# Optimization experiments

Hardware: AMD Instinct MI355X
Metric: run time of the kernel (lower is better)

The kernel has to match this reference:

```python
import jax, jax.numpy as jnp
import numpy as np

B, R, C = 2, 64, 256
PH = PW = 7
KMAX = 8            # max pool-kernel size per axis given roi size bounds (kernel<=7 here)
HW = [160, 80, 40, 20]   # FPN level spatial sizes for a 640px image, strides 4/8/16/32
STRIDES = [4.0, 8.0, 16.0, 32.0]
TOP = 224.0         # config.top_pyramid_roi_size
HIDDEN = 2048
NCLS = 20
SCALE = float(np.round(np.sqrt(C), 2))  # np.round(sqrt(inner_dim),2) in SelfAttention


def setup_inputs() -> dict:
    key = jax.random.key(0)
    ks = jax.random.split(key, 32)
    U = lambda k, s, lo, hi: jax.random.uniform(k, s, minval=lo, maxval=hi)
    x1 = U(ks[0], (B, R), 0.0, 260.0)
    y1 = U(ks[1], (B, R), 0.0, 260.0)
    w = U(ks[2], (B, R), 16.0, 360.0)
    h = U(ks[3], (B, R), 16.0, 360.0)
    rois = jnp.stack([x1, y1, jnp.minimum(x1 + w, 639.0), jnp.minimum(y1 + h, 639.0)], -1)
    N = lambda k, s, sc: (sc * jax.random.normal(k, s)).astype(jnp.float32)
    inp = {'rois': rois}
    for i in range(4):
        inp[f'fm{i}'] = N(ks[4 + i], (B, C, HW[i], HW[i]), 1.0)
    inp['wq'] = N(ks[8], (C, C), 0.02);  inp['bq'] = jnp.zeros((C,), jnp.float32)
    inp['wk'] = N(ks[9], (C, C), 0.02);  inp['bk'] = jnp.zeros((C,), jnp.float32)
    inp['wv'] = N(ks[10], (C, C), 0.02); inp['bv'] = jnp.zeros((C,), jnp.float32)
    inp['wo'] = N(ks[11], (C, C), 0.02); inp['bo'] = jnp.zeros((C,), jnp.float32)
    inp['w1'] = N(ks[12], (C * PH * PW, HIDDEN), 0.02); inp['b1'] = jnp.zeros((HIDDEN,), jnp.float32)
    inp['w2'] = N(ks[13], (HIDDEN, HIDDEN), 0.02);       inp['b2'] = jnp.zeros((HIDDEN,), jnp.float32)
    inp['wreg'] = N(ks[14], (HIDDEN, 4 * (NCLS + 1)), 0.02); inp['breg'] = jnp.zeros((4 * (NCLS + 1),), jnp.float32)
    inp['wcls'] = N(ks[15], (HIDDEN, NCLS + 1), 0.02);       inp['bcls'] = jnp.zeros((NCLS + 1,), jnp.float32)
    return inp


def _forward(rois, fm0, fm1, fm2, fm3, wq, bq, wk, bk, wv, bv, wo, bo,
             w1, b1, w2, b2, wreg, breg, wcls, bcls):
    Hmax = HW[0]
    pad = lambda fm: jnp.pad(fm, ((0, 0), (0, 0), (0, Hmax - fm.shape[-2]), (0, Hmax - fm.shape[-1])))
    feats = jnp.stack([pad(fm0), pad(fm1), pad(fm2), pad(fm3)])  # [4,B,C,Hmax,Hmax]
    heights = jnp.array(HW, jnp.int32)
    strides = jnp.array(STRIDES, jnp.float32)

    r = rois.reshape(-1, 4)                 # [N,4] xyxy in pixels
    Nroi = r.shape[0]
    bidx = jnp.repeat(jnp.arange(B, dtype=jnp.int32), R)
    size = jnp.sqrt((r[:, 2] - r[:, 0]) * (r[:, 3] - r[:, 1]))
    # int() truncates toward zero, then clamp(0,3) -- matches torch
    lvl = jnp.clip((3.0 + jnp.log(size / TOP)).astype(jnp.int32), 0, 3)
    s = strides[lvl]
    x1 = (r[:, 0] / s).astype(jnp.int32); y1 = (r[:, 1] / s).astype(jnp.int32)
    x2 = (r[:, 2] / s).astype(jnp.int32); y2 = (r[:, 3] / s).astype(jnp.int32)
    Hl = heights[lvl]                        # per-roi level map size (square maps)

    def expand(lo, hi, cap, pool):
        # replicate the symmetric while-loop expansion until span >= pool
        for _ in range(pool):
            need = (hi - lo + 1) < pool
            lo = jnp.where(need, jnp.maximum(lo - 1, 0), lo)
            hi = jnp.where(need, jnp.minimum(hi + 1, cap - 1), hi)
        return lo, hi

    y1, y2 = expand(y1, y2, Hl, PH)
    x1, x2 = expand(x1, x2, Hl, PW)
    rh = y2 - y1 + 1; rw = x2 - x1 + 1
    kh = (rh + PH - 1) // PH; sh = rh // PH   # ceil / floor kernel & stride
    kw = (rw + PW - 1) // PW; sw = rw // PW

    ar_p = jnp.arange(PH); ar_k = jnp.arange(KMAX)

    def pool_one(l, b, yy, xx, kh_, kw_, sh_, sw_):
        rows = jnp.clip(yy + ar_p[:, None] * sh_ + ar_k[None, :], 0, Hmax - 1)  # [PH,K]
        cols = jnp.clip(xx + ar_p[:, None] * sw_ + ar_k[None, :], 0, Hmax - 1)  # [PW,K]
        patch = feats[l, b][:, rows[:, :, None, None], cols[None, None, :, :]]  # [C,PH,K,PW,K]
        m = (ar_k < kh_)[:, None, None] & (ar_k < kw_)[None, None, :]           # [K,1,K] -> bcast
        patch = jnp.where(m, patch, -jnp.inf)
        return patch.max(axis=(2, 4))                                           # [C,PH,PW]

    pooled = jax.vmap(pool_one)(lvl, bidx, y1, x1, kh, kw, sh, sw)  # [N,C,PH,PW]

    # SelfAttention over the PH*PW spatial tokens of each ROI
    L = PH * PW
    tok = pooled.reshape(Nroi, C, L).transpose(0, 2, 1)            # [N,L,C]
    q = tok @ wq + bq
    k = tok @ wk + bk
    v = tok @ wv + bv
    att = jax.nn.softmax(jnp.einsum('nlc,nmc->nlm', q, k) / SCALE, axis=-1)
    ctx = jnp.einsum('nlm,nmc->nlc', att, v) @ wo + bo             # [N,L,C]
    x = pooled.reshape(Nroi, C, L) + ctx.transpose(0, 2, 1)        # residual add
    x = x.reshape(Nroi, C * L)

    h1 = jax.nn.relu(x @ w1 + b1)
    h2 = jax.nn.relu(h1 @ w2 + b2)
    bbox_reg = h2 @ wreg + breg                                    # [N, 4*(NCLS+1)]
    bbox_classes = jax.nn.softmax(h2 @ wcls + bcls, axis=-1)       # [N, NCLS+1]
    return bbox_reg, bbox_classes


def reference(rois, fm0, fm1, fm2, fm3, wq, bq, wk, bk, wv, bv, wo, bo,
              w1, b1, w2, b2, wreg, breg, wcls, bcls):
    return _forward(rois, fm0, fm1, fm2, fm3, wq, bq, wk, bk, wv, bv, wo, bo,
                    w1, b1, w2, b2, wreg, breg, wcls, bcls)
```

## Files before the change

### kernel.cpp

```cpp
#include <hip/hip_runtime.h>
#include <hip/hip_bf16.h>
#include <stdint.h>

typedef __attribute__((ext_vector_type(8))) short bf16x8;
typedef __attribute__((ext_vector_type(4))) float f32x4;

__device__ __forceinline__ float blo(unsigned u){ union{float f;unsigned x;}v; v.x = u<<16; return v.f; }
__device__ __forceinline__ float bhi(unsigned u){ union{float f;unsigned x;}v; v.x = u & 0xFFFF0000u; return v.f; }
__device__ __forceinline__ unsigned short f2bf(float f){
  union{float f;unsigned x;}v; v.f=f; unsigned x=v.x;
  return (unsigned short)((x + 0x7fffu + ((x>>16)&1u)) >> 16);
}
__device__ __forceinline__ unsigned cvtpk(float lo, float hi){
  unsigned r;
  asm("v_cvt_pk_bf16_f32 %0, %1, %2" : "=v"(r) : "v"(lo), "v"(hi));
  return r;
}
__device__ __forceinline__ void gll16(const float* g, float* l){
  __builtin_amdgcn_global_load_lds(
      (const __attribute__((address_space(1))) unsigned int*)g,
      (__attribute__((address_space(3))) unsigned int*)l, 16, 0, 0);
}

__global__ __launch_bounds__(256) void pool_pack_kernel(
    const float* __restrict__ rois,
    const float* __restrict__ fm0, const float* __restrict__ fm1,
    const float* __restrict__ fm2, const float* __restrict__ fm3,
    float* __restrict__ pooled, unsigned short* __restrict__ tok,
    const float* __restrict__ wreg, const float* __restrict__ wcls, float* __restrict__ wT)
{
  int bx = blockIdx.x;
  int tid = threadIdx.x;
  if (bx >= 896){
    int c = bx - 896;
    if (c < 84){
      for (int k = tid; k < 2048; k += 256) wT[(size_t)c*2048 + k] = wreg[(size_t)k*84 + c];
    } else {
      int cc = c - 84;
      for (int k = tid; k < 2048; k += 256) wT[(size_t)c*2048 + k] = wcls[(size_t)k*21 + cc];
    }
    return;
  }
  int n = bx / 7;
  int ph = bx - n*7;
  int c = tid;
  const float* r = rois + n*4;
  int b = n >> 6;
  float rx1=r[0], ry1=r[1], rx2=r[2], ry2=r[3];
  float size = sqrtf((rx2-rx1)*(ry2-ry1));
  int lvl = (int)(3.0f + logf(size/224.0f));
  if (lvl < 0) lvl = 0; if (lvl > 3) lvl = 3;
  const float strides_[4] = {4.f,8.f,16.f,32.f};
  const int hw_[4] = {160,80,40,20};
  float s = strides_[lvl]; int Hl = hw_[lvl];
  int x1 = (int)(rx1/s), y1 = (int)(ry1/s), x2 = (int)(rx2/s), y2 = (int)(ry2/s);
  #pragma unroll
  for (int it=0; it<7; ++it){
    bool need = (y2-y1+1) < 7;
    if (need){ y1 = (y1-1 > 0) ? y1-1 : 0; y2 = (y2+1 < Hl-1) ? y2+1 : Hl-1; }
  }
  #pragma unroll
  for (int it=0; it<7; ++it){
    bool need = (x2-x1+1) < 7;
    if (need){ x1 = (x1-1 > 0) ? x1-1 : 0; x2 = (x2+1 < Hl-1) ? x2+1 : Hl-1; }
  }
  int rh = y2-y1+1, rw = x2-x1+1;
  int kh = (rh+6)/7, sh = rh/7, kw = (rw+6)/7, sw2 = rw/7;
  const float* fm = (lvl==0)?fm0:(lvl==1)?fm1:(lvl==2)?fm2:fm3;
  const float* fp = fm + ((size_t)(b*256 + c))*(size_t)(Hl*Hl);
  int r0 = y1 + ph*sh;
  for (int pw=0; pw<7; ++pw){
    int c0 = x1 + pw*sw2;
    float m = -3.4e38f;
    for (int i=0;i<kh;++i){
      const float* rp = fp + (size_t)(r0+i)*Hl + c0;
      for (int j=0;j<kw;++j) m = fmaxf(m, rp[j]);
    }
    int l = ph*7+pw;
    pooled[((size_t)n*49 + l)*256 + c] = m;
    tok[((size_t)n*49 + l)*256 + c] = f2bf(m);
  }
}

template<bool GATHER>
__global__ __launch_bounds__(256) void fc_kernel(
    const unsigned short* __restrict__ A, const float* __restrict__ B,
    float* __restrict__ outf, int M, int K, int kChunk)
{
  __shared__ __align__(16) float Bs[4][32][64];
  int bid = blockIdx.x;
  int pe = gridDim.x >> 3;
  bid = (bid & 7)*pe + (bid >> 3);
  const int per = 64;
  int kc = bid / per;
  int rem = bid - kc*per;
  int bm = rem & 1, bn = rem >> 1;
  int m0 = bm*64, n0 = bn*64;
  int tid = threadIdx.x, lane = tid & 63, wave = tid >> 6;
  int wm = wave & 1, wn = wave >> 1;
  int g = lane >> 4, c = lane & 15;
  int k0 = kc*kChunk;
  int nSteps = kChunk >> 5;

  f32x4 acc[2][2];
  #pragma unroll
  for (int i=0;i<2;++i)
    #pragma unroll
    for (int j=0;j<2;++j){ acc[i][j][0]=0.f; acc[i][j][1]=0.f; acc[i][j][2]=0.f; acc[i][j][3]=0.f; }

  int rowInWave = lane >> 4;
  int colOff = n0 + (lane & 15)*4;
  const unsigned short* Ap0 = A + (size_t)(m0 + wm*32 +      c)*K + g*8;
  const unsigned short* Ap1 = A + (size_t)(m0 + wm*32 + 16 + c)*K + g*8;

  auto srcRow = [&](int k)->const float*{
    if constexpr (GATHER){ int kk = k; return B + ((size_t)((kk & 255)*49 + (kk >> 8)))*2048; }
    else                 { return B + (size_t)k*2048; }
  };
  auto stage = [&](int buf, int kk){
    int r0a = kk + wave*8 + rowInWave;
    int r0b = r0a + 4;
    gll16(srcRow(r0a) + colOff, &Bs[buf][wave*8    ][0]);
    gll16(srcRow(r0b) + colOff, &Bs[buf][wave*8 + 4][0]);
  };

  stage(0, k0); stage(1, k0+32); stage(2, k0+64);
  uint4 aCur0 = *(const uint4*)(Ap0 + k0);
  uint4 aCur1 = *(const uint4*)(Ap1 + k0);

  for (int i = 0; i < nSteps; ++i){
    int kk = k0 + (i<<5);
    int pend = nSteps - i;
    if (pend >= 3)      asm volatile("s_waitcnt vmcnt(4)" ::: "memory");
    else if (pend == 2) asm volatile("s_waitcnt vmcnt(2)" ::: "memory");
    else                asm volatile("s_waitcnt vmcnt(0)" ::: "memory");
    __builtin_amdgcn_s_barrier();

    uint4 aNxt0 = aCur0, aNxt1 = aCur1;
    if (i+1 < nSteps){
      aNxt0 = *(const uint4*)(Ap0 + kk + 32);
      aNxt1 = *(const uint4*)(Ap1 + kk + 32);
    }
    if (i+3 < nSteps) stage((i+3)&3, kk + 96);

    const float* fb = &Bs[i&3][g*8][wn*32 + c];
    float q0f[8], q1f[8];
    #pragma unroll
    for (int j=0;j<8;++j){ q0f[j] = fb[j*64]; q1f[j] = fb[j*64 + 16]; }
    union { unsigned u[4]; bf16x8 v; } q0u, q1u;
    q0u.u[0]=cvtpk(q0f[0],q0f[1]); q0u.u[1]=cvtpk(q0f[2],q0f[3]);
    q0u.u[2]=cvtpk(q0f[4],q0f[5]); q0u.u[3]=cvtpk(q0f[6],q0f[7]);
    q1u.u[0]=cvtpk(q1f[0],q1f[1]); q1u.u[1]=cvtpk(q1f[2],q1f[3]);
    q1u.u[2]=cvtpk(q1f[4],q1f[5]); q1u.u[3]=cvtpk(q1f[6],q1f[7]);
    bf16x8 f0 = *(const bf16x8*)&aCur0;
    bf16x8 f1 = *(const bf16x8*)&aCur1;
    acc[0][0] = __builtin_amdgcn_mfma_f32_16x16x32_bf16(f0,q0u.v,acc[0][0],0,0,0);
    acc[0][1] = __builtin_amdgcn_mfma_f32_16x16x32_bf16(f0,q1u.v,acc[0][1],0,0,0);
    acc[1][0] = __builtin_amdgcn_mfma_f32_16x16x32_bf16(f1,q0u.v,acc[1][0],0,0,0);
    acc[1][1] = __builtin_amdgcn_mfma_f32_16x16x32_bf16(f1,q1u.v,acc[1][1],0,0,0);
    aCur0 = aNxt0; aCur1 = aNxt1;
  }

  int rq = g << 2;
  #pragma unroll
  for (int mr=0;mr<2;++mr){
    #pragma unroll
    for (int nc=0;nc<2;++nc){
      int rowb = m0 + wm*32 + mr*16 + rq;
      int colM = n0 + wn*32 + nc*16 + c;
      #pragma unroll
      for (int r2=0;r2<4;++r2){
        outf[(size_t)kc*M*2048 + (size_t)(rowb+r2)*2048 + colM] = acc[mr][nc][r2];
      }
    }
  }
}

template<int EPI>
__global__ __launch_bounds__(256) void gemm_kernel(
    const unsigned short* __restrict__ A,
    const float* __restrict__ B0, const float* __restrict__ B1, const float* __restrict__ B2,
    const float* __restrict__ bias0, const float* __restrict__ bias1, const float* __restrict__ bias2,
    unsigned short* __restrict__ o0, unsigned short* __restrict__ o1, unsigned short* __restrict__ o2,
    const float* __restrict__ pooled,
    int M, int Nper, int K, int nM, int nN, int kChunk)
{
  __shared__ __align__(16) unsigned short Bs[2][2048];
  int bid = blockIdx.x;
  int tid = threadIdx.x;
  int per = nM*nN;
  int kc  = bid / per;
  int rem = bid - kc*per;
  int bm = rem % nM, bn = rem / nM;
  int m0 = bm*64, n0 = bn*64;
  int mat = n0 / Nper;
  int col0 = n0 - mat*Nper;
  const float* Bp    = (mat==0)?B0:(mat==1)?B1:B2;
  const float* biasp = (mat==0)?bias0:(mat==1)?bias1:bias2;
  unsigned short* outp = (mat==0)?o0:(mat==1)?o1:o2;
  int k0 = kc*kChunk;
  int nMacro = kChunk >> 7;
  int lane = tid & 63, wave = tid >> 6;
  int wm = wave & 1, wn = wave >> 1;
  int g = lane >> 4, c = lane & 15;

  f32x4 acc[2][2];
  #pragma unroll
  for (int i=0;i<2;++i)
    #pragma unroll
    for (int j=0;j<2;++j){ acc[i][j][0]=0.f; acc[i][j][1]=0.f; acc[i][j][2]=0.f; acc[i][j][3]=0.f; }

  int brow = tid >> 3, bcg = tid & 7;
  int bw_idx = brow*64 + ((bcg*8) ^ ((brow>>3)<<4));
  const float* Bbase = Bp + (size_t)brow*Nper + col0 + bcg*8;
  int rb0 = g*512 + (((wn*2  )^g)*16 + c);
  int rb1 = g*512 + (((wn*2+1)^g)*16 + c);
  const unsigned short* Ap0 = A + (size_t)(m0 + wm*32 +      c)*K + g*8;
  const unsigned short* Ap1 = A + (size_t)(m0 + wm*32 + 16 + c)*K + g*8;

  auto writeB = [&](int buf, const float4& bx, const float4& by){
    uint4 w;
    w.x = cvtpk(bx.x,bx.y); w.y = cvtpk(bx.z,bx.w);
    w.z = cvtpk(by.x,by.y); w.w = cvtpk(by.z,by.w);
    *(uint4*)&Bs[buf][bw_idx] = w;
  };
  auto readFrags = [&](int buf, bf16x8& r0, bf16x8& r1){
    union { unsigned short s[8]; bf16x8 v; } u0, u1;
    const unsigned short* bsp = &Bs[buf][0];
    #pragma unroll
    for (int j=0;j<8;++j){ u0.s[j] = bsp[rb0 + j*64]; u1.s[j] = bsp[rb1 + j*64]; }
    r0 = u0.v; r1 = u1.v;
  };
  auto mfma4 = [&](const bf16x8& f0, const bf16x8& f1, const bf16x8& q0, const bf16x8& q1){
    acc[0][0] = __builtin_amdgcn_mfma_f32_16x16x32_bf16(f0,q0,acc[0][0],0,0,0);
    acc[0][1] = __builtin_amdgcn_mfma_f32_16x16x32_bf16(f0,q1,acc[0][1],0,0,0);
    acc[1][0] = __builtin_amdgcn_mfma_f32_16x16x32_bf16(f1,q0,acc[1][0],0,0,0);
    acc[1][1] = __builtin_amdgcn_mfma_f32_16x16x32_bf16(f1,q1,acc[1][1],0,0,0);
  };

  for (int mi = 0; mi < nMacro; ++mi){
    int kk = k0 + (mi << 7);
    uint4 a0x = *(const uint4*)(Ap0+kk),    a0y = *(const uint4*)(Ap1+kk);
    uint4 a1x = *(const uint4*)(Ap0+kk+32), a1y = *(const uint4*)(Ap1+kk+32);
    uint4 a2x = *(const uint4*)(Ap0+kk+64), a2y = *(const uint4*)(Ap1+kk+64);
    uint4 a3x = *(const uint4*)(Ap0+kk+96), a3y = *(const uint4*)(Ap1+kk+96);
    const float* p0 = Bbase + (size_t)kk*Nper;
    const float* p1 = p0 + (size_t)32*Nper;
    const float* p2 = p0 + (size_t)64*Nper;
    const float* p3 = p0 + (size_t)96*Nper;
    float4 b0a = *(const float4*)p0, b0b = *(const float4*)(p0+4);
    float4 b1a = *(const float4*)p1, b1b = *(const float4*)(p1+4);
    float4 b2a = *(const float4*)p2, b2b = *(const float4*)(p2+4);
    float4 b3a = *(const float4*)p3, b3b = *(const float4*)(p3+4);

    writeB(0, b0a, b0b);
    __syncthreads();
    bf16x8 q0,q1;
    readFrags(0,q0,q1);
    writeB(1,b1a,b1b);
    mfma4(*(const bf16x8*)&a0x, *(const bf16x8*)&a0y, q0,q1);
    __syncthreads();
    readFrags(1,q0,q1);
    writeB(0,b2a,b2b);
    mfma4(*(const bf16x8*)&a1x, *(const bf16x8*)&a1y, q0,q1);
    __syncthreads();
    readFrags(0,q0,q1);
    writeB(1,b3a,b3b);
    mfma4(*(const bf16x8*)&a2x, *(const bf16x8*)&a2y, q0,q1);
    __syncthreads();
    readFrags(1,q0,q1);
    mfma4(*(const bf16x8*)&a3x, *(const bf16x8*)&a3y, q0,q1);
  }

  int rq = g << 2, cl = c;
  #pragma unroll
  for (int mr=0;mr<2;++mr){
    #pragma unroll
    for (int nc=0;nc<2;++nc){
      int rowb = m0 + wm*32 + mr*16 + rq;
      int colM = col0 + wn*32 + nc*16 + cl;
      #pragma unroll
      for (int r2=0;r2<4;++r2){
        float v = acc[mr][nc][r2];
        int rr = rowb + r2;
        if constexpr (EPI==0){
          v += biasp[colM];
          outp[(size_t)rr*Nper + colM] = f2bf(v);
        } else {
          v += biasp[colM];
          v += pooled[(size_t)rr*256 + colM];
          int nn = rr/49, l = rr - nn*49;
          outp[(size_t)nn*12544 + l*256 + colM] = f2bf(v);
        }
      }
    }
  }
}

__global__ __launch_bounds__(256) void reduce1_kernel(
    const float* __restrict__ part, const float* __restrict__ b1,
    unsigned short* __restrict__ h1, int nPart)
{
  int i = blockIdx.x*256 + threadIdx.x;
  float4 s = ((const float4*)part)[i];
  for (int kc = 1; kc < nPart; ++kc){
    float4 p = ((const float4*)part)[(size_t)kc*65536 + i];
    s.x += p.x; s.y += p.y; s.z += p.z; s.w += p.w;
  }
  float4 bb = *(const float4*)(b1 + ((i<<2) & 2047));
  s.x = fmaxf(s.x+bb.x,0.f); s.y = fmaxf(s.y+bb.y,0.f);
  s.z = fmaxf(s.z+bb.z,0.f); s.w = fmaxf(s.w+bb.w,0.f);
  uint2 w;
  w.x = cvtpk(s.x, s.y); w.y = cvtpk(s.z, s.w);
  *(uint2*)&h1[(size_t)i<<2] = w;
}

__global__ __launch_bounds__(256) void reduce2_kernel(
    const float* __restrict__ part, float* __restrict__ h2f, int nPart)
{
  int i = blockIdx.x*256 + threadIdx.x;
  float4 s = ((const float4*)part)[i];
  for (int kc = 1; kc < nPart; ++kc){
    float4 p = ((const float4*)part)[(size_t)kc*65536 + i];
    s.x += p.x; s.y += p.y; s.z += p.z; s.w += p.w;
  }
  ((float4*)h2f)[i] = s;
}

__global__ __launch_bounds__(256) void attn_kernel(
    const unsigned short* __restrict__ Q, const unsigned short* __restrict__ Km,
    const unsigned short* __restrict__ V, unsigned short* __restrict__ ctx)
{
  int n = blockIdx.x, half = blockIdx.y, tid = threadIdx.x;
  int r0 = half*25, rcnt = half ? 24 : 25;
  __shared__ __align__(16) unsigned short qs[25*256];
  __shared__ __align__(16) unsigned short ks[49*260];
  __shared__ float S[25*49];
  const uint4* qg = (const uint4*)(Q + ((size_t)n*49 + r0)*256);
  for (int i = tid; i < rcnt*32; i += 256) ((uint4*)qs)[i] = qg[i];
  const uint2* kg = (const uint2*)(Km + (size_t)n*49*256);
  for (int i = tid; i < 49*64; i += 256){
    int j = i >> 6, s = i & 63;
    *(uint2*)(ks + j*260 + s*4) = kg[i];
  }
  __syncthreads();
  for (int p = tid; p < rcnt*49; p += 256){
    int i = p/49, j = p - i*49;
    const uint2* qr = (const uint2*)(qs + i*256);
    const uint2* kr = (const uint2*)(ks + j*260);
    float sum = 0.f;
    #pragma unroll 8
    for (int c4 = 0; c4 < 64; ++c4){
      uint2 qv = qr[c4], kv = kr[c4];
      sum += blo(qv.x)*blo(kv.x) + bhi(qv.x)*bhi(kv.x);
      sum += blo(qv.y)*blo(kv.y) + bhi(qv.y)*bhi(kv.y);
    }
    S[p] = sum * (1.0f/16.0f);
  }
  __syncthreads();
  const uint2* vg = (const uint2*)(V + (size_t)n*49*256);
  for (int i = tid; i < 49*64; i += 256){
    int j = i >> 6, s = i & 63;
    *(uint2*)(ks + j*260 + s*4) = vg[i];
  }
  if (tid < rcnt){
    float* row = S + tid*49;
    float mx = row[0];
    for (int j=1;j<49;++j) mx = fmaxf(mx,row[j]);
    float sm = 0.f;
    for (int j=0;j<49;++j){ float e = expf(row[j]-mx); row[j]=e; sm+=e; }
    float inv = 1.0f/sm;
    for (int j=0;j<49;++j) row[j] *= inv;
  }
  __syncthreads();
  for (int idx = tid; idx < rcnt*64; idx += 256){
    int i = idx >> 6, cp4 = idx & 63;
    const float* att = S + i*49;
    float s0=0.f, s1=0.f, s2=0.f, s3=0.f;
    #pragma unroll 7
    for (int j=0;j<49;++j){
      uint2 v = *(const uint2*)(ks + j*260 + cp4*4);
      float a = att[j];
      s0 += a*blo(v.x); s1 += a*bhi(v.x);
      s2 += a*blo(v.y); s3 += a*bhi(v.y);
    }
    uint2 outw;
    outw.x = (unsigned)f2bf(s0) | ((unsigned)f2bf(s1) << 16);
    outw.y = (unsigned)f2bf(s2) | ((unsigned)f2bf(s3) << 16);
    *(uint2*)&ctx[((size_t)n*49 + r0 + i)*256 + cp4*4] = outw;
  }
}

__global__ __launch_bounds__(256) void heads_dot(
    const float* __restrict__ h2f, const float* __restrict__ b2,
    const float* __restrict__ wT,
    const float* __restrict__ breg, const float* __restrict__ bcls,
    float* __restrict__ out, float* __restrict__ logits)
{
  int gw = (blockIdx.x*256 + threadIdx.x) >> 6;
  int lane = threadIdx.x & 63;
  int m = gw / 105, c = gw - m*105;
  const float4* hp = (const float4*)(h2f + (size_t)m*2048);
  const float4* bp = (const float4*)b2;
  const float4* wp = (const float4*)(wT + (size_t)c*2048);
  float sum = 0.f;
  #pragma unroll
  for (int i=0;i<8;++i){
    float4 a = hp[i*64 + lane];
    float4 bb = bp[i*64 + lane];
    float4 w = wp[i*64 + lane];
    sum += fmaxf(a.x+bb.x,0.f)*w.x + fmaxf(a.y+bb.y,0.f)*w.y
         + fmaxf(a.z+bb.z,0.f)*w.z + fmaxf(a.w+bb.w,0.f)*w.w;
  }
  #pragma unroll
  for (int off=32; off; off>>=1) sum += __shfl_down(sum, off, 64);
  if (lane == 0){
    if (c < 84) out[(size_t)m*84 + c] = sum + breg[c];
    else        logits[(size_t)m*21 + (c-84)] = sum + bcls[c-84];
  }
}

__global__ __launch_bounds__(128) void cls_softmax(
    const float* __restrict__ logits, float* __restrict__ out)
{
  int m = threadIdx.x;
  const float* lg = logits + (size_t)m*21;
  float mx = lg[0];
  #pragma unroll
  for (int j=1;j<21;++j) mx = fmaxf(mx, lg[j]);
  float sm = 0.f;
  float e[21];
  #pragma unroll
  for (int j=0;j<21;++j){ e[j] = expf(lg[j]-mx); sm += e[j]; }
  float inv = 1.0f/sm;
  #pragma unroll
  for (int j=0;j<21;++j) out[10752 + (size_t)m*21 + j] = e[j]*inv;
}

extern "C" void kernel_launch(void* const* d_in, const int* in_sizes, int n_in,
                              void* d_out, int out_size, void* d_ws, size_t ws_size,
                              hipStream_t stream)
{
  (void)in_sizes; (void)n_in; (void)out_size; (void)ws_size;
  const float* rois = (const float*)d_in[0];
  const float* fm0  = (const float*)d_in[1];
  const float* fm1  = (const float*)d_in[2];
  const float* fm2  = (const float*)d_in[3];
  const float* fm3  = (const float*)d_in[4];
  const float* wq   = (const float*)d_in[5];
  const float* bq   = (const float*)d_in[6];
  const float* wk   = (const float*)d_in[7];
  const float* bk   = (const float*)d_in[8];
  const float* wv   = (const float*)d_in[9];
  const float* bv   = (const float*)d_in[10];
  const float* wo   = (const float*)d_in[11];
  const float* bo   = (const float*)d_in[12];
  const float* w1   = (const float*)d_in[13];
  const float* b1   = (const float*)d_in[14];
  const float* w2   = (const float*)d_in[15];
  const float* b2   = (const float*)d_in[16];
  const float* wreg = (const float*)d_in[17];
  const float* breg = (const float*)d_in[18];
  const float* wcls = (const float*)d_in[19];
  const float* bcls = (const float*)d_in[20];
  float* out = (float*)d_out;

  char* ws = (char*)d_ws;
  float*          pooled = (float*)(ws + 0);
  unsigned short* tok    = (unsigned short*)(ws + 6422528);
  unsigned short* Qb     = (unsigned short*)(ws + 9633792);
  unsigned short* Kb     = (unsigned short*)(ws + 12845056);
  unsigned short* Vb     = (unsigned short*)(ws + 16056320);
  unsigned short* ctx    = (unsigned short*)(ws + 19267584);
  unsigned short* xb     = (unsigned short*)(ws + 22478848);
  float*          h2f    = (float*)(ws + 25690112);
  unsigned short* h1     = (unsigned short*)(ws + 26738688);
  float*          wT     = (float*)(ws + 27787264);
  float*          logits = (float*)(ws + 28647424);
  float*          h1part = (float*)(ws + 29360128);
  float*          h2part = (float*)(ws + 29360128);

  pool_pack_kernel<<<1001,256,0,stream>>>(rois, fm0, fm1, fm2, fm3, pooled, tok,
                                          wreg, wcls, wT);

  gemm_kernel<0><<<1176,256,0,stream>>>(tok, wq,wk,wv, bq,bk,bv,
                                        Qb,Kb,Vb, nullptr,
                                        6272,256,256, 98,12, 256);

  attn_kernel<<<dim3(128,2),256,0,stream>>>(Qb, Kb, Vb, ctx);

  gemm_kernel<1><<<392,256,0,stream>>>(ctx, wo,wo,wo, bo,bo,bo,
                                       xb,xb,xb, pooled,
                                       6272,256,256, 98,4, 256);

  fc_kernel<true><<<1792,256,0,stream>>>(xb, w1, h1part, 128, 12544, 448);
  reduce1_kernel<<<256,256,0,stream>>>(h1part, b1, h1, 28);

  fc_kernel<false><<<1024,256,0,stream>>>(h1, w2, h2part, 128, 2048, 128);
  reduce2_kernel<<<256,256,0,stream>>>(h2part, h2f, 16);

  heads_dot<<<3360,256,0,stream>>>(h2f, b2, wT, breg, bcls, out, logits);
  cls_softmax<<<1,128,0,stream>>>(logits, out);
}
```

Baseline: 161.6 us.

## Pre-convert FC weights to bf16 and stage bf16 tiles in fc_kernel

Adds extra blocks to the pooling kernel that convert w1 and w2 from fp32 to bf16 into workspace on every call. fc_kernel then stages bf16 tiles through LDS with one global-to-LDS load per lane and no per-step cvt_pk packing, which halves its LDS footprint. The first FC also doubles its K chunk, giving half as many split-K partials to reduce. The cost is a full extra read and write of the large weight matrices each call, which may outweigh the cheaper GEMM loads.

```diff
diff --git a/kernel.cpp b/kernel.cpp
--- a/kernel.cpp
+++ b/kernel.cpp
@@ -16,7 +16,7 @@
   asm("v_cvt_pk_bf16_f32 %0, %1, %2" : "=v"(r) : "v"(lo), "v"(hi));
   return r;
 }
-__device__ __forceinline__ void gll16(const float* g, float* l){
+__device__ __forceinline__ void gll16s(const unsigned short* g, unsigned short* l){
   __builtin_amdgcn_global_load_lds(
       (const __attribute__((address_space(1))) unsigned int*)g,
       (__attribute__((address_space(3))) unsigned int*)l, 16, 0, 0);
@@ -27,10 +27,26 @@
     const float* __restrict__ fm0, const float* __restrict__ fm1,
     const float* __restrict__ fm2, const float* __restrict__ fm3,
     float* __restrict__ pooled, unsigned short* __restrict__ tok,
-    const float* __restrict__ wreg, const float* __restrict__ wcls, float* __restrict__ wT)
+    const float* __restrict__ wreg, const float* __restrict__ wcls, float* __restrict__ wT,
+    const float* __restrict__ w1, unsigned short* __restrict__ w1b,
+    const float* __restrict__ w2, unsigned short* __restrict__ w2b)
 {
   int bx = blockIdx.x;
   int tid = threadIdx.x;
+  if (bx >= 1001){
+    int z = bx - 1001;
+    const int total = (12544 + 2048) * 512;
+    for (int idx = z*256 + tid; idx < total; idx += 1024*256){
+      int row = idx >> 9, col4 = idx & 511;
+      const float* src; unsigned short* dst;
+      if (row < 12544){ src = w1 + (size_t)row*2048; dst = w1b + (size_t)row*2048; }
+      else { int r2 = row - 12544; src = w2 + (size_t)r2*2048; dst = w2b + (size_t)r2*2048; }
+      float4 v = *(const float4*)(src + col4*4);
+      uint2 w; w.x = cvtpk(v.x, v.y); w.y = cvtpk(v.z, v.w);
+      *(uint2*)(dst + col4*4) = w;
+    }
+    return;
+  }
   if (bx >= 896){
     int c = bx - 896;
     if (c < 84){
@@ -84,10 +100,10 @@
 
 template<bool GATHER>
 __global__ __launch_bounds__(256) void fc_kernel(
-    const unsigned short* __restrict__ A, const float* __restrict__ B,
+    const unsigned short* __restrict__ A, const unsigned short* __restrict__ B,
     float* __restrict__ outf, int M, int K, int kChunk)
 {
-  __shared__ __align__(16) float Bs[4][32][64];
+  __shared__ __align__(16) unsigned short Bs[4][32][64];
   int bid = blockIdx.x;
   int pe = gridDim.x >> 3;
   bid = (bid & 7)*pe + (bid >> 3);
@@ -108,20 +124,17 @@
     #pragma unroll
     for (int j=0;j<2;++j){ acc[i][j][0]=0.f; acc[i][j][1]=0.f; acc[i][j][2]=0.f; acc[i][j][3]=0.f; }
 
-  int rowInWave = lane >> 4;
-  int colOff = n0 + (lane & 15)*4;
+  int rowSel = lane >> 3;
+  int colSel = (lane & 7) * 8;
   const unsigned short* Ap0 = A + (size_t)(m0 + wm*32 +      c)*K + g*8;
   const unsigned short* Ap1 = A + (size_t)(m0 + wm*32 + 16 + c)*K + g*8;
 
-  auto srcRow = [&](int k)->const float*{
-    if constexpr (GATHER){ int kk = k; return B + ((size_t)((kk & 255)*49 + (kk >> 8)))*2048; }
-    else                 { return B + (size_t)k*2048; }
+  auto srcRow = [&](int k)->const unsigned short*{
+    if constexpr (GATHER) return B + ((size_t)((k & 255)*49 + (k >> 8)))*2048;
+    else                  return B + (size_t)k*2048;
   };
   auto stage = [&](int buf, int kk){
-    int r0a = kk + wave*8 + rowInWave;
-    int r0b = r0a + 4;
-    gll16(srcRow(r0a) + colOff, &Bs[buf][wave*8    ][0]);
-    gll16(srcRow(r0b) + colOff, &Bs[buf][wave*8 + 4][0]);
+    gll16s(srcRow(kk + wave*8 + rowSel) + n0 + colSel, &Bs[buf][wave*8][0]);
   };
 
   stage(0, k0); stage(1, k0+32); stage(2, k0+64);
@@ -143,15 +156,10 @@
     }
     if (i+3 < nSteps) stage((i+3)&3, kk + 96);
 
-    const float* fb = &Bs[i&3][g*8][wn*32 + c];
-    float q0f[8], q1f[8];
+    const unsigned short* fb = &Bs[i&3][g*8][wn*32 + c];
+    union { unsigned short s[8]; bf16x8 v; } q0u, q1u;
     #pragma unroll
-    for (int j=0;j<8;++j){ q0f[j] = fb[j*64]; q1f[j] = fb[j*64 + 16]; }
-    union { unsigned u[4]; bf16x8 v; } q0u, q1u;
-    q0u.u[0]=cvtpk(q0f[0],q0f[1]); q0u.u[1]=cvtpk(q0f[2],q0f[3]);
-    q0u.u[2]=cvtpk(q0f[4],q0f[5]); q0u.u[3]=cvtpk(q0f[6],q0f[7]);
-    q1u.u[0]=cvtpk(q1f[0],q1f[1]); q1u.u[1]=cvtpk(q1f[2],q1f[3]);
-    q1u.u[2]=cvtpk(q1f[4],q1f[5]); q1u.u[3]=cvtpk(q1f[6],q1f[7]);
+    for (int j=0;j<8;++j){ q0u.s[j] = fb[j*64]; q1u.s[j] = fb[j*64 + 16]; }
     bf16x8 f0 = *(const bf16x8*)&aCur0;
     bf16x8 f1 = *(const bf16x8*)&aCur1;
     acc[0][0] = __builtin_amdgcn_mfma_f32_16x16x32_bf16(f0,q0u.v,acc[0][0],0,0,0);
@@ -477,11 +485,13 @@
   unsigned short* h1     = (unsigned short*)(ws + 26738688);
   float*          wT     = (float*)(ws + 27787264);
   float*          logits = (float*)(ws + 28647424);
-  float*          h1part = (float*)(ws + 29360128);
-  float*          h2part = (float*)(ws + 29360128);
-
-  pool_pack_kernel<<<1001,256,0,stream>>>(rois, fm0, fm1, fm2, fm3, pooled, tok,
-                                          wreg, wcls, wT);
+  unsigned short* w1b    = (unsigned short*)(ws + 29360128);
+  unsigned short* w2b    = (unsigned short*)(ws + 80740352);
+  float*          h1part = (float*)(ws + 0);
+  float*          h2part = (float*)(ws + 0);
+
+  pool_pack_kernel<<<2025,256,0,stream>>>(rois, fm0, fm1, fm2, fm3, pooled, tok,
+                                          wreg, wcls, wT, w1, w1b, w2, w2b);
 
   gemm_kernel<0><<<1176,256,0,stream>>>(tok, wq,wk,wv, bq,bk,bv,
                                         Qb,Kb,Vb, nullptr,
@@ -493,10 +503,10 @@
                                        xb,xb,xb, pooled,
                                        6272,256,256, 98,4, 256);
 
-  fc_kernel<true><<<1792,256,0,stream>>>(xb, w1, h1part, 128, 12544, 448);
-  reduce1_kernel<<<256,256,0,stream>>>(h1part, b1, h1, 28);
-
-  fc_kernel<false><<<1024,256,0,stream>>>(h1, w2, h2part, 128, 2048, 128);
+  fc_kernel<true><<<896,256,0,stream>>>(xb, w1b, h1part, 128, 12544, 896);
+  reduce1_kernel<<<256,256,0,stream>>>(h1part, b1, h1, 14);
+
+  fc_kernel<false><<<1024,256,0,stream>>>(h1, w2b, h2part, 128, 2048, 128);
   reduce2_kernel<<<256,256,0,stream>>>(h2part, h2f, 16);
 
   heads_dot<<<3360,256,0,stream>>>(h2f, b2, wT, breg, bcls, out, logits);
```

Result: slower. 185.7 us (+14.9%).
